# Kernel tuning notes

Hardware: AMD Instinct MI355X
Metric: run time of the kernel (lower is better)

Reference implementation:

```python
import jax, jax.numpy as jnp
import numpy as np

N_KNN = 16
BN_EPS = 1e-5


def conv1d(x, w, b):
    # x: [B, Cin, N], w: [Cout, Cin], b: [Cout] (1x1 Conv1d)
    return jnp.einsum('oc,bcn->bon', w, x) + b[None, :, None]


def conv2d(x, w, b):
    # x: [B, Cin, N, K], w: [Cout, Cin], b: [Cout] (1x1 Conv2d)
    return jnp.einsum('oc,bcnk->bonk', w, x) + b[None, :, None, None]


def bn2d(x, gamma, beta, mean, var):
    # eval-mode BatchNorm2d over channel axis 1
    scale = (gamma / jnp.sqrt(var + BN_EPS))[None, :, None, None]
    return (x - mean[None, :, None, None]) * scale + beta[None, :, None, None]


def knn_idx(pos, k):
    # pos: [B, 3, N] -> idx: [B, N, K] of k nearest neighbors (incl. self)
    p = jnp.swapaxes(pos, 1, 2)  # [B, N, 3]
    sq = jnp.sum(p * p, axis=-1)  # [B, N]
    d2 = sq[:, :, None] - 2.0 * jnp.einsum('bnd,bmd->bnm', p, p) + sq[:, None, :]
    _, idx = jax.lax.top_k(-d2, k)
    return idx


def group(x, idx):
    # x: [B, C, N], idx: [B, N, K] -> [B, C, N, K] (grouping_operation)
    return jax.vmap(lambda xb, ib: xb[:, ib])(x, idx)


def setup_inputs() -> dict:
    key = jax.random.key(0)
    B, C_OBJ, C_Q, N, DIM, PH, AM = 4, 512, 512, 4096, 128, 64, 4
    ks = jax.random.split(key, 32)
    r = lambda i, sh, s=0.05: jax.random.normal(ks[i], sh, jnp.float32) * s
    inp = {
        'obj_feature': jax.random.normal(ks[0], (B, C_OBJ, N), jnp.float32),
        'pos': jax.random.normal(ks[1], (B, 3, N), jnp.float32),
        'query_points': jax.random.normal(ks[2], (B, C_Q, N), jnp.float32),
        # linear_start_query / linear_start_obj
        'w_sq': r(3, (DIM, C_Q)), 'b_sq': r(4, (DIM,)),
        'w_so': r(5, (DIM, C_OBJ)), 'b_so': r(6, (DIM,)),
        # key / query / value 1x1 convs
        'w_k': r(7, (DIM, DIM)), 'b_k': r(8, (DIM,)),
        'w_q': r(9, (DIM, DIM)), 'b_q': r(10, (DIM,)),
        'w_v': r(11, (DIM, DIM)), 'b_v': r(12, (DIM,)),
        # pos_mlp: Conv2d(3->PH), BN, ReLU, Conv2d(PH->DIM)
        'w_p1': r(13, (PH, 3)), 'b_p1': r(14, (PH,)),
        'g_bn1': 1.0 + r(15, (PH,)), 'be_bn1': r(16, (PH,)),
        'm_bn1': r(17, (PH,)), 'v_bn1': 1.0 + 0.1 * jax.random.uniform(ks[18], (PH,), jnp.float32),
        'w_p2': r(19, (DIM, PH)), 'b_p2': r(20, (DIM,)),
        # attn_mlp: Conv2d(DIM->DIM*AM), BN, ReLU, Conv2d(DIM*AM->DIM)
        'w_a1': r(21, (DIM * AM, DIM)), 'b_a1': r(22, (DIM * AM,)),
        'g_bn2': 1.0 + r(23, (DIM * AM,)), 'be_bn2': r(24, (DIM * AM,)),
        'm_bn2': r(25, (DIM * AM,)), 'v_bn2': 1.0 + 0.1 * jax.random.uniform(ks[26], (DIM * AM,), jnp.float32),
        # linear_end
        'w_e': r(27, (C_OBJ, DIM)), 'b_e': r(28, (C_OBJ,)),
    }
    return inp


def reference(obj_feature, pos, query_points, w_sq, b_sq, w_so, b_so, w_k, b_k,
              w_q, b_q, w_v, b_v, w_p1, b_p1, g_bn1, be_bn1, m_bn1, v_bn1,
              w_p2, b_p2, w_a1, b_a1, g_bn2, be_bn2, m_bn2, v_bn2, w_e, b_e):
    qf = conv1d(query_points, w_sq, b_sq)          # [B, dim, N]
    f = conv1d(obj_feature, w_so, b_so)            # [B, dim, N]
    idx = knn_idx(jax.lax.stop_gradient(pos), N_KNN)  # [B, N, K]
    key_g = group(conv1d(f, w_k, b_k), idx)        # [B, dim, N, K]
    value = conv1d(f, w_v, b_v)                    # [B, dim, N]
    query = conv1d(qf, w_q, b_q)                   # [B, dim, N]
    qk_rel = query[:, :, :, None] - key_g          # [B, dim, N, K]
    pos_rel = pos[:, :, :, None] - group(pos, idx)  # [B, 3, N, K]
    pe = conv2d(jax.nn.relu(bn2d(conv2d(pos_rel, w_p1, b_p1), g_bn1, be_bn1, m_bn1, v_bn1)), w_p2, b_p2)
    attn = conv2d(jax.nn.relu(bn2d(conv2d(qk_rel + pe, w_a1, b_a1), g_bn2, be_bn2, m_bn2, v_bn2)), w_a2_placeholder := w_p2 * 0 + 0, b_p2 * 0) if False else None
    hidden = jax.nn.relu(bn2d(conv2d(qk_rel + pe, w_a1, b_a1), g_bn2, be_bn2, m_bn2, v_bn2))
    attn = jax.nn.softmax(conv2d(hidden, w_a2, b_a2), axis=-1)  # softmax over K
    v = value[:, :, :, None] + pe                  # [B, dim, N, K]
    agg = jnp.sum(attn * v, axis=-1)               # 'b c i j, b c i j -> b c i'
    return conv1d(agg, w_e, b_e)                   # [B, C_obj, N]

# fix: w_a2/b_a2 are parameters; re-declare reference cleanly to include them

def _setup_extra(inp):
    kk = jax.random.split(jax.random.key(7), 2)
    inp['w_a2'] = jax.random.normal(kk[0], (128, 512), jnp.float32) * 0.05
    inp['b_a2'] = jax.random.normal(kk[1], (128,), jnp.float32) * 0.05
    return inp

_orig_setup = setup_inputs

def setup_inputs():
    return _setup_extra(_orig_setup())


def reference(obj_feature, pos, query_points, w_sq, b_sq, w_so, b_so, w_k, b_k,
              w_q, b_q, w_v, b_v, w_p1, b_p1, g_bn1, be_bn1, m_bn1, v_bn1,
              w_p2, b_p2, w_a1, b_a1, g_bn2, be_bn2, m_bn2, v_bn2, w_a2, b_a2,
              w_e, b_e):
    qf = conv1d(query_points, w_sq, b_sq)
    f = conv1d(obj_feature, w_so, b_so)
    idx = knn_idx(jax.lax.stop_gradient(pos), N_KNN)
    key_g = group(conv1d(f, w_k, b_k), idx)
    value = conv1d(f, w_v, b_v)
    query = conv1d(qf, w_q, b_q)
    qk_rel = query[:, :, :, None] - key_g
    pos_rel = pos[:, :, :, None] - group(pos, idx)
    pe = conv2d(jax.nn.relu(bn2d(conv2d(pos_rel, w_p1, b_p1), g_bn1, be_bn1, m_bn1, v_bn1)), w_p2, b_p2)
    hidden = jax.nn.relu(bn2d(conv2d(qk_rel + pe, w_a1, b_a1), g_bn2, be_bn2, m_bn2, v_bn2))
    attn = jax.nn.softmax(conv2d(hidden, w_a2, b_a2), axis=-1)
    v = value[:, :, :, None] + pe
    agg = jnp.sum(attn * v, axis=-1)
    return conv1d(agg, w_e, b_e)
```

## Files before the change

### kernel.cpp

```cpp
#include <hip/hip_runtime.h>

typedef __bf16 bf16;
typedef __bf16 bf16x8 __attribute__((ext_vector_type(8)));
typedef __bf16 bf16x4 __attribute__((ext_vector_type(4)));
typedef __bf16 bf16x2 __attribute__((ext_vector_type(2)));
typedef float f32x4 __attribute__((ext_vector_type(4)));

#define MFMA16(a,b,c) __builtin_amdgcn_mfma_f32_16x16x32_bf16((a),(b),(c),0,0,0)

#define NPTS 4096
#define CIN 512
#define DIM 128
#define PH 64
#define HID 512

#define OFF_WQS 0u
#define OFF_WKO (128u*1024u)
#define OFF_WVO (256u*1024u)
#define OFF_BQS (384u*1024u)
#define OFF_BKO (385u*1024u)
#define OFF_BVO (386u*1024u)
#define OFF_S1  (387u*1024u)
#define OFF_T1  (388u*1024u)
#define OFF_S2  (389u*1024u)
#define OFF_T2  (391u*1024u)
#define OFF_CW  (400u*1024u)
#define OFF_QT  (1u<<20)
#define OFF_KT  (OFF_QT + (4u<<20))
#define OFF_VT  (OFF_QT + (8u<<20))
#define OFF_IDX (OFF_QT + (12u<<20))
#define WS_NEED (OFF_QT + (13u<<20))

struct P {
  const float* in[31];
  char* ws;
  float* out;
  int ybase;
};

template<int C> __device__ __forceinline__ float rorf(float x){
  return __int_as_float(__builtin_amdgcn_mov_dpp(__float_as_int(x), 0x120|C, 0xF, 0xF, true));
}
__device__ __forceinline__ float red16max(float x){
  x=fmaxf(x,rorf<1>(x)); x=fmaxf(x,rorf<2>(x)); x=fmaxf(x,rorf<4>(x)); x=fmaxf(x,rorf<8>(x)); return x;
}
__device__ __forceinline__ float red16sum(float x){
  x+=rorf<1>(x); x+=rorf<2>(x); x+=rorf<4>(x); x+=rorf<8>(x); return x;
}
template<int C> __device__ __forceinline__ unsigned long long ror64(unsigned long long k){
  unsigned lo = (unsigned)__builtin_amdgcn_mov_dpp((int)(unsigned)k,        0x120|C, 0xF, 0xF, true);
  unsigned hi = (unsigned)__builtin_amdgcn_mov_dpp((int)(unsigned)(k>>32), 0x120|C, 0xF, 0xF, true);
  return ((unsigned long long)hi<<32)|lo;
}

__global__ __launch_bounds__(256) void k_fold(P p) {
  int tid = blockIdx.x*256 + threadIdx.x;
  char* ws = p.ws;
  if (tid < 196608) {
    int m_id = tid >> 16, o = (tid >> 9) & 127, c = tid & 511;
    const float* A  = m_id==0 ? p.in[9] : (m_id==1 ? p.in[7] : p.in[11]);
    const float* Bm = (m_id==0) ? p.in[3] : p.in[5];
    float acc = 0.f;
    #pragma unroll 8
    for (int m=0;m<128;m++) acc += A[o*128+m] * Bm[m*512+c];
    bf16* outw = (bf16*)(ws + (m_id==0?OFF_WQS: m_id==1?OFF_WKO:OFF_WVO));
    outw[o*512+c] = (bf16)acc;
  } else if (tid < 196992) {
    int t = tid - 196608; int m_id = t >> 7, o = t & 127;
    const float* A  = m_id==0 ? p.in[9] : (m_id==1 ? p.in[7] : p.in[11]);
    const float* bb = (m_id==0) ? p.in[4] : p.in[6];
    const float* bs = m_id==0 ? p.in[10] : (m_id==1 ? p.in[8] : p.in[12]);
    float acc = bs[o];
    for (int m=0;m<128;m++) acc += A[o*128+m] * bb[m];
    float* ob = (float*)(ws + (m_id==0?OFF_BQS: m_id==1?OFF_BKO:OFF_BVO));
    ob[o] = acc;
  } else if (tid < 197056) {
    int i = tid - 196992;
    float s = p.in[15][i] * rsqrtf(p.in[18][i] + 1e-5f);
    ((float*)(ws+OFF_S1))[i] = s;
    ((float*)(ws+OFF_T1))[i] = (p.in[14][i] - p.in[17][i])*s + p.in[16][i];
  } else if (tid < 197568) {
    int i = tid - 197056;
    float s = p.in[23][i] * rsqrtf(p.in[26][i] + 1e-5f);
    ((float*)(ws+OFF_S2))[i] = s;
    ((float*)(ws+OFF_T2))[i] = (p.in[22][i] - p.in[25][i])*s + p.in[24][i];
  } else if (tid < 223168) {
    int e0 = (tid - 197568) * 8;
    const float* src; int base;
    if (e0 < 8192)        { src = p.in[19]; base = 0; }
    else if (e0 < 73728)  { src = p.in[21]; base = 8192; }
    else if (e0 < 139264) { src = p.in[29]; base = 73728; }
    else                  { src = p.in[27]; base = 139264; }
    const float* sp = src + (e0 - base);
    f32x4 a = *(const f32x4*)sp, b2 = *(const f32x4*)(sp+4);
    bf16x8 o8;
    o8[0]=(bf16)a[0]; o8[1]=(bf16)a[1]; o8[2]=(bf16)a[2]; o8[3]=(bf16)a[3];
    o8[4]=(bf16)b2[0]; o8[5]=(bf16)b2[1]; o8[6]=(bf16)b2[2]; o8[7]=(bf16)b2[3];
    *(bf16x8*)((bf16*)(ws+OFF_CW) + e0) = o8;
  }
}

__global__ __launch_bounds__(256) void k_knn(P p) {
  int lane = threadIdx.x & 63, w = threadIdx.x >> 6;
  int ig = blockIdx.x*4 + w;
  int b = ig >> 12, n = ig & 4095;
  const float* pb = p.in[1] + b*3*NPTS;
  float qx = pb[n], qy = pb[NPTS+n], qz = pb[2*NPTS+n];
  float sqn = __fadd_rn(__fadd_rn(__fmul_rn(qx,qx), __fmul_rn(qy,qy)), __fmul_rn(qz,qz));
  unsigned u[64];
  #pragma unroll
  for (int t=0;t<64;t++) {
    int j = t*64 + lane;
    float xj=pb[j], yj=pb[NPTS+j], zj=pb[2*NPTS+j];
    float sqj = __fadd_rn(__fadd_rn(__fmul_rn(xj,xj), __fmul_rn(yj,yj)), __fmul_rn(zj,zj));
    float dot = __fadd_rn(__fadd_rn(__fmul_rn(qx,xj), __fmul_rn(qy,yj)), __fmul_rn(qz,zj));
    float d2 = __fadd_rn(__fsub_rn(sqn, __fmul_rn(2.f,dot)), sqj);
    unsigned bb2 = __float_as_uint(d2);
    u[t] = bb2 ^ (((unsigned)((int)bb2 >> 31)) | 0x80000000u);
  }
  unsigned v0=u[0], v1=u[16], v2=u[32], v3=u[48];
  int t0=0, t1=16, t2=32, t3=48;
  #pragma unroll
  for (int i=1;i<16;i++) {
    { bool lt=u[i]    <v0; v0=lt?u[i]   :v0; t0=lt?(i)   :t0; }
    { bool lt=u[16+i] <v1; v1=lt?u[16+i]:v1; t1=lt?(16+i):t1; }
    { bool lt=u[32+i] <v2; v2=lt?u[32+i]:v2; t2=lt?(32+i):t2; }
    { bool lt=u[48+i] <v3; v3=lt?u[48+i]:v3; t3=lt?(48+i):t3; }
  }
  int* op = (int*)(p.ws + OFF_IDX) + ig*16;
  #pragma unroll 1
  for (int r=0;r<16;r++) {
    unsigned va=v0; int ta=t0;
    { bool lt=v1<va; va=lt?v1:va; ta=lt?t1:ta; }
    unsigned vb=v2; int tb=t2;
    { bool lt=v3<vb; vb=lt?v3:vb; tb=lt?t3:tb; }
    { bool lt=vb<va; va=lt?vb:va; ta=lt?tb:ta; }
    unsigned long long key = ((unsigned long long)va << 12) | (unsigned)((ta<<6) | lane);
    { unsigned long long o = ror64<1>(key); if (o<key) key=o; }
    { unsigned long long o = ror64<2>(key); if (o<key) key=o; }
    { unsigned long long o = ror64<4>(key); if (o<key) key=o; }
    { unsigned long long o = ror64<8>(key); if (o<key) key=o; }
    { unsigned long long o = __shfl_xor(key,16); if (o<key) key=o; }
    { unsigned long long o = __shfl_xor(key,32); if (o<key) key=o; }
    unsigned jwin = (unsigned)key & 4095u;
    if (lane==0) op[r] = (int)jwin;
    if (r==15) break;
    int tsel = __builtin_amdgcn_readfirstlane((int)(jwin>>6));
    bool mine = ((int)(jwin&63)==lane);
    switch (tsel) {
#define CLR(T) case T: u[T] = mine ? 0xFFFFFFFFu : u[T]; break;
      CLR(0) CLR(1) CLR(2) CLR(3) CLR(4) CLR(5) CLR(6) CLR(7)
      CLR(8) CLR(9) CLR(10) CLR(11) CLR(12) CLR(13) CLR(14) CLR(15)
      CLR(16) CLR(17) CLR(18) CLR(19) CLR(20) CLR(21) CLR(22) CLR(23)
      CLR(24) CLR(25) CLR(26) CLR(27) CLR(28) CLR(29) CLR(30) CLR(31)
      CLR(32) CLR(33) CLR(34) CLR(35) CLR(36) CLR(37) CLR(38) CLR(39)
      CLR(40) CLR(41) CLR(42) CLR(43) CLR(44) CLR(45) CLR(46) CLR(47)
      CLR(48) CLR(49) CLR(50) CLR(51) CLR(52) CLR(53) CLR(54) CLR(55)
      CLR(56) CLR(57) CLR(58) CLR(59) CLR(60) CLR(61) CLR(62) CLR(63)
#undef CLR
      default: break;
    }
    switch (tsel >> 4) {
      case 0: { v0=u[0]; t0=0;
        #pragma unroll
        for (int i=1;i<16;i++){ bool lt=u[i]<v0; v0=lt?u[i]:v0; t0=lt?i:t0; } } break;
      case 1: { v1=u[16]; t1=16;
        #pragma unroll
        for (int i=1;i<16;i++){ bool lt=u[16+i]<v1; v1=lt?u[16+i]:v1; t1=lt?(16+i):t1; } } break;
      case 2: { v2=u[32]; t2=32;
        #pragma unroll
        for (int i=1;i<16;i++){ bool lt=u[32+i]<v2; v2=lt?u[32+i]:v2; t2=lt?(32+i):t2; } } break;
      default: { v3=u[48]; t3=48;
        #pragma unroll
        for (int i=1;i<16;i++){ bool lt=u[48+i]<v3; v3=lt?u[48+i]:v3; t3=lt?(48+i):t3; } } break;
    }
  }
}

__global__ __launch_bounds__(256) void k_qkv(P p) {
  int mat = blockIdx.z, b = blockIdx.y, n0 = blockIdx.x*64;
  int tid = threadIdx.x, lane = tid&63, w = tid>>6;
  const float* in = (mat==0 ? p.in[2] : p.in[0]) + b*CIN*NPTS;
  const bf16* W = (const bf16*)(p.ws + (mat==0?OFF_WQS: mat==1?OFF_WKO:OFF_WVO));
  const float* bias = (const float*)(p.ws + (mat==0?OFF_BQS: mat==1?OFF_BKO:OFF_BVO));
  bf16* outT = (bf16*)(p.ws + (mat==0?OFF_QT: mat==1?OFF_KT:OFF_VT)) + (b*NPTS + n0)*DIM;
  __shared__ __align__(16) bf16 Bl[64*40];
  f32x4 acc[8] = {};
  for (int ks=0; ks<16; ks++) {
    int c0 = ks*32;
    {
      int cc = tid>>3, nn0 = (tid&7)*8;
      const float* sp = in + (c0+cc)*NPTS + n0 + nn0;
      f32x4 a = *(const f32x4*)sp, b2 = *(const f32x4*)(sp+4);
      Bl[(nn0+0)*40+cc]=(bf16)a[0];  Bl[(nn0+1)*40+cc]=(bf16)a[1];
      Bl[(nn0+2)*40+cc]=(bf16)a[2];  Bl[(nn0+3)*40+cc]=(bf16)a[3];
      Bl[(nn0+4)*40+cc]=(bf16)b2[0]; Bl[(nn0+5)*40+cc]=(bf16)b2[1];
      Bl[(nn0+6)*40+cc]=(bf16)b2[2]; Bl[(nn0+7)*40+cc]=(bf16)b2[3];
    }
    __syncthreads();
    int ncol = w*16 + (lane&15);
    bf16x8 bfr = *(const bf16x8*)(&Bl[ncol*40 + (lane>>4)*8]);
    #pragma unroll
    for (int ot=0;ot<8;ot++) {
      bf16x8 af = *(const bf16x8*)(W + (ot*16 + (lane&15))*CIN + c0 + (lane>>4)*8);
      acc[ot] = MFMA16(af, bfr, acc[ot]);
    }
    __syncthreads();
  }
  int o0 = (lane>>4)*4;
  int nloc = w*16 + (lane&15);
  #pragma unroll
  for (int ot=0;ot<8;ot++) {
    f32x4 bs = *(const f32x4*)(bias + ot*16 + o0);
    bf16x4 st;
    st[0]=(bf16)(acc[ot][0]+bs[0]); st[1]=(bf16)(acc[ot][1]+bs[1]);
    st[2]=(bf16)(acc[ot][2]+bs[2]); st[3]=(bf16)(acc[ot][3]+bs[3]);
    *(bf16x4*)(outT + nloc*DIM + ot*16 + o0) = st;
  }
}

__global__ __launch_bounds__(512) void k_fused(P p) {
  int bb = p.ybase + blockIdx.y, pt0 = blockIdx.x*8;
  int tid=threadIdx.x, lane=tid&63, w=tid>>6;
  int c = lane&15, g = lane>>4;
  char* ws = p.ws;
  const bf16* qT = (const bf16*)(ws+OFF_QT) + bb*NPTS*DIM;
  const bf16* kT = (const bf16*)(ws+OFF_KT) + bb*NPTS*DIM;
  const bf16* vT = (const bf16*)(ws+OFF_VT) + bb*NPTS*DIM;
  const int* idxg = (const int*)(ws+OFF_IDX) + (bb*NPTS + pt0)*16;
  const bf16* wp2b = (const bf16*)(ws+OFF_CW);
  const bf16* wa1b = wp2b + 8192;
  const bf16* wa2b = wa1b + 65536;
  const bf16* web  = wa2b + 65536;
  const float* s2 = (const float*)(ws+OFF_S2);
  const float* t2 = (const float*)(ws+OFF_T2);
  __shared__ __align__(16) char LB[53248];
  bf16* Xl = (bf16*)LB;
  bf16* HT = (bf16*)(LB + 34816);
  bf16* aggl = (bf16*)(LB + 34816);

  {
    int col = w*16 + c;
    int j = idxg[col] & 4095;
    const float* pb = p.in[1] + bb*3*NPTS;
    int n = pt0 + w;
    float r0 = pb[n]-pb[j], r1 = pb[NPTS+n]-pb[NPTS+j], r2 = pb[2*NPTS+n]-pb[2*NPTS+j];
    const float* wp1 = p.in[13];
    const float* s1 = (const float*)(ws+OFF_S1);
    const float* t1 = (const float*)(ws+OFF_T1);
    #pragma unroll
    for (int i=0;i<16;i+=2) {
      int m = g*16 + i;
      float x0 = wp1[m*3]*r0   + wp1[m*3+1]*r1 + wp1[m*3+2]*r2;
      float x1 = wp1[m*3+3]*r0 + wp1[m*3+4]*r1 + wp1[m*3+5]*r2;
      bf16x2 pk;
      pk[0] = (bf16)fmaxf(0.f, x0*s1[m]   + t1[m]);
      pk[1] = (bf16)fmaxf(0.f, x1*s1[m+1] + t1[m+1]);
      *(bf16x2*)(&HT[col*72 + m]) = pk;
    }
  }
  __syncthreads();

  {
    f32x4 acc[8] = {};
    int crow = w*16 + c;
    #pragma unroll
    for (int ksx=0; ksx<2; ksx++) {
      int m0 = ksx*32 + g*8;
      bf16x8 af = *(const bf16x8*)(wp2b + crow*PH + m0);
      #pragma unroll
      for (int nt=0; nt<8; nt++) {
        int col = nt*16 + c;
        bf16x8 bfr = *(const bf16x8*)(&HT[col*72 + m0]);
        acc[nt] = MFMA16(af, bfr, acc[nt]);
      }
    }
    int c0 = w*16 + g*4;
    f32x4 bp4 = *(const f32x4*)(p.in[20] + c0);
    #pragma unroll
    for (int nt=0; nt<8; nt++) {
      int col = nt*16 + c;
      int j = idxg[col] & 4095;
      int n = pt0 + nt;
      bf16x4 q4 = *(const bf16x4*)(qT + n*DIM + c0);
      bf16x4 k4 = *(const bf16x4*)(kT + j*DIM + c0);
      bf16x4 st;
      #pragma unroll
      for (int r=0;r<4;r++)
        st[r] = (bf16)((float)q4[r] - (float)k4[r] + acc[nt][r] + bp4[r]);
      *(bf16x4*)(&Xl[col*136 + c0]) = st;
    }
  }
  __syncthreads();

  int mh = w & 1, nc1 = w >> 1;
  int wo = w & 3, wc = w >> 2;
  f32x4 S[2][4] = {{{},{},{},{}},{{},{},{},{}}};
  for (int ch=0; ch<8; ch++) {
    f32x4 acc1[2][2] = {{{},{}},{{},{}}};
    #pragma unroll
    for (int ksx=0; ksx<4; ksx++) {
      int k0 = ksx*32 + g*8;
      bf16x8 af0 = *(const bf16x8*)(wa1b + (ch*64 + mh*32 + c)*DIM + k0);
      bf16x8 af1 = *(const bf16x8*)(wa1b + (ch*64 + mh*32 + 16 + c)*DIM + k0);
      bf16x8 b0  = *(const bf16x8*)(&Xl[(nc1*32 + c)*136 + k0]);
      bf16x8 b1  = *(const bf16x8*)(&Xl[(nc1*32 + 16 + c)*136 + k0]);
      acc1[0][0] = MFMA16(af0, b0, acc1[0][0]);
      acc1[0][1] = MFMA16(af0, b1, acc1[0][1]);
      acc1[1][0] = MFMA16(af1, b0, acc1[1][0]);
      acc1[1][1] = MFMA16(af1, b1, acc1[1][1]);
    }
    #pragma unroll
    for (int i2=0;i2<2;i2++) {
      int hl = mh*32 + i2*16 + g*4;
      int hg = ch*64 + hl;
      f32x4 sv = *(const f32x4*)(s2 + hg);
      f32x4 tv = *(const f32x4*)(t2 + hg);
      #pragma unroll
      for (int j2=0;j2<2;j2++) {
        int col = nc1*32 + j2*16 + c;
        bf16x4 st;
        st[0]=(bf16)fmaxf(0.f, acc1[i2][j2][0]*sv[0]+tv[0]);
        st[1]=(bf16)fmaxf(0.f, acc1[i2][j2][1]*sv[1]+tv[1]);
        st[2]=(bf16)fmaxf(0.f, acc1[i2][j2][2]*sv[2]+tv[2]);
        st[3]=(bf16)fmaxf(0.f, acc1[i2][j2][3]*sv[3]+tv[3]);
        *(bf16x4*)(&HT[col*72 + hl]) = st;
      }
    }
    __syncthreads();
    #pragma unroll
    for (int ksx=0; ksx<2; ksx++) {
      int k0 = ksx*32 + g*8;
      bf16x8 af0 = *(const bf16x8*)(wa2b + (wo*32 + c)*HID + ch*64 + k0);
      bf16x8 af1 = *(const bf16x8*)(wa2b + (wo*32 + 16 + c)*HID + ch*64 + k0);
      #pragma unroll
      for (int n2=0;n2<4;n2++) {
        bf16x8 bfr = *(const bf16x8*)(&HT[(wc*64 + n2*16 + c)*72 + k0]);
        S[0][n2] = MFMA16(af0, bfr, S[0][n2]);
        S[1][n2] = MFMA16(af1, bfr, S[1][n2]);
      }
    }
    __syncthreads();
  }

  {
    #pragma unroll
    for (int n2=0;n2<4;n2++) {
      int ptl = wc*4 + n2;
      int colg = ptl*16 + c;
      int j = idxg[colg] & 4095;
      int n = pt0 + ptl;
      #pragma unroll
      for (int i2=0;i2<2;i2++) {
        int chb = wo*32 + i2*16 + g*4;
        bf16x4 x4 = *(const bf16x4*)(&Xl[colg*136 + chb]);
        bf16x4 q4 = *(const bf16x4*)(qT + n*DIM + chb);
        bf16x4 k4 = *(const bf16x4*)(kT + j*DIM + chb);
        bf16x4 v4 = *(const bf16x4*)(vT + n*DIM + chb);
        float agv[4];
        #pragma unroll
        for (int r=0;r<4;r++) {
          float s = S[i2][n2][r];
          float mx = red16max(s);
          float e = __expf(s-mx);
          float sm = red16sum(e);
          float at = e/sm;
          float vpe = (float)v4[r] + (float)x4[r] - (float)q4[r] + (float)k4[r];
          agv[r] = red16sum(at*vpe);
        }
        if (c==0) {
          bf16x4 st; st[0]=(bf16)agv[0]; st[1]=(bf16)agv[1]; st[2]=(bf16)agv[2]; st[3]=(bf16)agv[3];
          *(bf16x4*)(&aggl[ptl*136 + chb]) = st;
        }
      }
    }
  }
  __syncthreads();

  {
    const float* be = p.in[28];
    f32x4 acc5[4] = {};
    #pragma unroll
    for (int ksx=0; ksx<4; ksx++) {
      bf16x8 bfr = *(const bf16x8*)(&aggl[c*136 + ksx*32 + g*8]);
      #pragma unroll
      for (int i=0;i<4;i++) {
        int e = (w*4+i)*16 + c;
        bf16x8 af = *(const bf16x8*)(web + e*DIM + ksx*32 + g*8);
        acc5[i] = MFMA16(af, bfr, acc5[i]);
      }
    }
    if (c < 8) {
      int n = pt0 + c;
      #pragma unroll
      for (int i=0;i<4;i++) {
        int e0 = (w*4+i)*16 + g*4;
        f32x4 be4 = *(const f32x4*)(be + e0);
        #pragma unroll
        for (int r=0;r<4;r++)
          p.out[(bb*CIN + e0+r)*NPTS + n] = acc5[i][r] + be4[r];
      }
    }
  }
}

extern "C" void kernel_launch(void* const* d_in, const int* in_sizes, int n_in,
                              void* d_out, int out_size, void* d_ws, size_t ws_size,
                              hipStream_t stream) {
  if (ws_size < WS_NEED || n_in < 31) return;
  P p;
  for (int i=0;i<31;i++) p.in[i] = (const float*)d_in[i];
  p.ws = (char*)d_ws;
  p.out = (float*)d_out;
  p.ybase = 0;
  k_fold<<<872, 256, 0, stream>>>(p);
  k_knn<<<4096, 256, 0, stream>>>(p);
  k_qkv<<<dim3(64, 4, 3), 256, 0, stream>>>(p);
  k_fused<<<dim3(512, 4), 512, 0, stream>>>(p);
}
```

Measured before the change: 476.0 us.

## Merge knn and qkv launches; halve fused tile to 4 points per block

The qkv projection blocks are folded into the knn kernel as a leading range of block indices, so both independent jobs share one launch and can overlap on the device. The fused attention kernel now handles 4 points (64 neighbor columns) per block instead of 8, with a reworked warp-to-tile mapping, 128-wide hidden chunks and a smaller LDS footprint (about 33KB instead of 52KB). This raises block count and occupancy, at the cost of loading the weights again for every block, twice as often overall.

```diff
diff --git a/kernel.cpp b/kernel.cpp
--- a/kernel.cpp
+++ b/kernel.cpp
@@ -100,9 +100,52 @@
   }
 }
 
-__global__ __launch_bounds__(256) void k_knn(P p) {
+__global__ __launch_bounds__(256) void k_knnqkv(P p) {
+  if (blockIdx.x < 768) {
+    int qb = blockIdx.x;
+    int mat = qb >> 8, b = (qb >> 6) & 3, n0 = (qb & 63) * 64;
+    int tid = threadIdx.x, lane = tid&63, w = tid>>6;
+    const float* in = (mat==0 ? p.in[2] : p.in[0]) + b*CIN*NPTS;
+    const bf16* W = (const bf16*)(p.ws + (mat==0?OFF_WQS: mat==1?OFF_WKO:OFF_WVO));
+    const float* bias = (const float*)(p.ws + (mat==0?OFF_BQS: mat==1?OFF_BKO:OFF_BVO));
+    bf16* outT = (bf16*)(p.ws + (mat==0?OFF_QT: mat==1?OFF_KT:OFF_VT)) + (b*NPTS + n0)*DIM;
+    __shared__ __align__(16) bf16 Bl[64*40];
+    f32x4 acc[8] = {};
+    for (int ks=0; ks<16; ks++) {
+      int c0 = ks*32;
+      {
+        int cc = tid>>3, nn0 = (tid&7)*8;
+        const float* sp = in + (c0+cc)*NPTS + n0 + nn0;
+        f32x4 a = *(const f32x4*)sp, b2 = *(const f32x4*)(sp+4);
+        Bl[(nn0+0)*40+cc]=(bf16)a[0];  Bl[(nn0+1)*40+cc]=(bf16)a[1];
+        Bl[(nn0+2)*40+cc]=(bf16)a[2];  Bl[(nn0+3)*40+cc]=(bf16)a[3];
+        Bl[(nn0+4)*40+cc]=(bf16)b2[0]; Bl[(nn0+5)*40+cc]=(bf16)b2[1];
+        Bl[(nn0+6)*40+cc]=(bf16)b2[2]; Bl[(nn0+7)*40+cc]=(bf16)b2[3];
+      }
+      __syncthreads();
+      int ncol = w*16 + (lane&15);
+      bf16x8 bfr = *(const bf16x8*)(&Bl[ncol*40 + (lane>>4)*8]);
+      #pragma unroll
+      for (int ot=0;ot<8;ot++) {
+        bf16x8 af = *(const bf16x8*)(W + (ot*16 + (lane&15))*CIN + c0 + (lane>>4)*8);
+        acc[ot] = MFMA16(af, bfr, acc[ot]);
+      }
+      __syncthreads();
+    }
+    int o0 = (lane>>4)*4;
+    int nloc = w*16 + (lane&15);
+    #pragma unroll
+    for (int ot=0;ot<8;ot++) {
+      f32x4 bs = *(const f32x4*)(bias + ot*16 + o0);
+      bf16x4 st;
+      st[0]=(bf16)(acc[ot][0]+bs[0]); st[1]=(bf16)(acc[ot][1]+bs[1]);
+      st[2]=(bf16)(acc[ot][2]+bs[2]); st[3]=(bf16)(acc[ot][3]+bs[3]);
+      *(bf16x4*)(outT + nloc*DIM + ot*16 + o0) = st;
+    }
+    return;
+  }
   int lane = threadIdx.x & 63, w = threadIdx.x >> 6;
-  int ig = blockIdx.x*4 + w;
+  int ig = (blockIdx.x - 768)*4 + w;
   int b = ig >> 12, n = ig & 4095;
   const float* pb = p.in[1] + b*3*NPTS;
   float qx = pb[n], qy = pb[NPTS+n], qz = pb[2*NPTS+n];
@@ -177,50 +220,8 @@
   }
 }
 
-__global__ __launch_bounds__(256) void k_qkv(P p) {
-  int mat = blockIdx.z, b = blockIdx.y, n0 = blockIdx.x*64;
-  int tid = threadIdx.x, lane = tid&63, w = tid>>6;
-  const float* in = (mat==0 ? p.in[2] : p.in[0]) + b*CIN*NPTS;
-  const bf16* W = (const bf16*)(p.ws + (mat==0?OFF_WQS: mat==1?OFF_WKO:OFF_WVO));
-  const float* bias = (const float*)(p.ws + (mat==0?OFF_BQS: mat==1?OFF_BKO:OFF_BVO));
-  bf16* outT = (bf16*)(p.ws + (mat==0?OFF_QT: mat==1?OFF_KT:OFF_VT)) + (b*NPTS + n0)*DIM;
-  __shared__ __align__(16) bf16 Bl[64*40];
-  f32x4 acc[8] = {};
-  for (int ks=0; ks<16; ks++) {
-    int c0 = ks*32;
-    {
-      int cc = tid>>3, nn0 = (tid&7)*8;
-      const float* sp = in + (c0+cc)*NPTS + n0 + nn0;
-      f32x4 a = *(const f32x4*)sp, b2 = *(const f32x4*)(sp+4);
-      Bl[(nn0+0)*40+cc]=(bf16)a[0];  Bl[(nn0+1)*40+cc]=(bf16)a[1];
-      Bl[(nn0+2)*40+cc]=(bf16)a[2];  Bl[(nn0+3)*40+cc]=(bf16)a[3];
-      Bl[(nn0+4)*40+cc]=(bf16)b2[0]; Bl[(nn0+5)*40+cc]=(bf16)b2[1];
-      Bl[(nn0+6)*40+cc]=(bf16)b2[2]; Bl[(nn0+7)*40+cc]=(bf16)b2[3];
-    }
-    __syncthreads();
-    int ncol = w*16 + (lane&15);
-    bf16x8 bfr = *(const bf16x8*)(&Bl[ncol*40 + (lane>>4)*8]);
-    #pragma unroll
-    for (int ot=0;ot<8;ot++) {
-      bf16x8 af = *(const bf16x8*)(W + (ot*16 + (lane&15))*CIN + c0 + (lane>>4)*8);
-      acc[ot] = MFMA16(af, bfr, acc[ot]);
-    }
-    __syncthreads();
-  }
-  int o0 = (lane>>4)*4;
-  int nloc = w*16 + (lane&15);
-  #pragma unroll
-  for (int ot=0;ot<8;ot++) {
-    f32x4 bs = *(const f32x4*)(bias + ot*16 + o0);
-    bf16x4 st;
-    st[0]=(bf16)(acc[ot][0]+bs[0]); st[1]=(bf16)(acc[ot][1]+bs[1]);
-    st[2]=(bf16)(acc[ot][2]+bs[2]); st[3]=(bf16)(acc[ot][3]+bs[3]);
-    *(bf16x4*)(outT + nloc*DIM + ot*16 + o0) = st;
-  }
-}
-
 __global__ __launch_bounds__(512) void k_fused(P p) {
-  int bb = p.ybase + blockIdx.y, pt0 = blockIdx.x*8;
+  int bb = blockIdx.y, pt0 = blockIdx.x*4;
   int tid=threadIdx.x, lane=tid&63, w=tid>>6;
   int c = lane&15, g = lane>>4;
   char* ws = p.ws;
@@ -234,144 +235,139 @@
   const bf16* web  = wa2b + 65536;
   const float* s2 = (const float*)(ws+OFF_S2);
   const float* t2 = (const float*)(ws+OFF_T2);
-  __shared__ __align__(16) char LB[53248];
+  __shared__ __align__(16) char LB[33792];
   bf16* Xl = (bf16*)LB;
-  bf16* HT = (bf16*)(LB + 34816);
-  bf16* aggl = (bf16*)(LB + 34816);
+  bf16* HT = (bf16*)(LB + 16896);
+  bf16* aggl = (bf16*)(LB + 16896);
 
   {
-    int col = w*16 + c;
+    int col = lane;
     int j = idxg[col] & 4095;
     const float* pb = p.in[1] + bb*3*NPTS;
-    int n = pt0 + w;
+    int n = pt0 + (col>>4);
     float r0 = pb[n]-pb[j], r1 = pb[NPTS+n]-pb[NPTS+j], r2 = pb[2*NPTS+n]-pb[2*NPTS+j];
     const float* wp1 = p.in[13];
     const float* s1 = (const float*)(ws+OFF_S1);
     const float* t1 = (const float*)(ws+OFF_T1);
-    #pragma unroll
-    for (int i=0;i<16;i+=2) {
-      int m = g*16 + i;
-      float x0 = wp1[m*3]*r0   + wp1[m*3+1]*r1 + wp1[m*3+2]*r2;
-      float x1 = wp1[m*3+3]*r0 + wp1[m*3+4]*r1 + wp1[m*3+5]*r2;
-      bf16x2 pk;
-      pk[0] = (bf16)fmaxf(0.f, x0*s1[m]   + t1[m]);
-      pk[1] = (bf16)fmaxf(0.f, x1*s1[m+1] + t1[m+1]);
-      *(bf16x2*)(&HT[col*72 + m]) = pk;
-    }
+    bf16x4 o4[2];
+    #pragma unroll
+    for (int i=0;i<8;i++) {
+      int m = w*8 + i;
+      float x = wp1[m*3]*r0 + wp1[m*3+1]*r1 + wp1[m*3+2]*r2;
+      o4[i>>2][i&3] = (bf16)fmaxf(0.f, x*s1[m] + t1[m]);
+    }
+    *(bf16x4*)(&HT[col*132 + w*8])     = o4[0];
+    *(bf16x4*)(&HT[col*132 + w*8 + 4]) = o4[1];
   }
   __syncthreads();
 
   {
-    f32x4 acc[8] = {};
-    int crow = w*16 + c;
+    f32x4 acc[4] = {};
+    int erow = w*16 + c;
     #pragma unroll
     for (int ksx=0; ksx<2; ksx++) {
       int m0 = ksx*32 + g*8;
-      bf16x8 af = *(const bf16x8*)(wp2b + crow*PH + m0);
-      #pragma unroll
-      for (int nt=0; nt<8; nt++) {
-        int col = nt*16 + c;
-        bf16x8 bfr = *(const bf16x8*)(&HT[col*72 + m0]);
-        acc[nt] = MFMA16(af, bfr, acc[nt]);
+      bf16x8 af = *(const bf16x8*)(wp2b + erow*PH + m0);
+      #pragma unroll
+      for (int ct=0; ct<4; ct++) {
+        bf16x8 bfr = *(const bf16x8*)(&HT[(ct*16+c)*132 + m0]);
+        acc[ct] = MFMA16(af, bfr, acc[ct]);
       }
     }
     int c0 = w*16 + g*4;
     f32x4 bp4 = *(const f32x4*)(p.in[20] + c0);
     #pragma unroll
-    for (int nt=0; nt<8; nt++) {
-      int col = nt*16 + c;
+    for (int ct=0; ct<4; ct++) {
+      int col = ct*16 + c;
       int j = idxg[col] & 4095;
-      int n = pt0 + nt;
+      int n = pt0 + ct;
       bf16x4 q4 = *(const bf16x4*)(qT + n*DIM + c0);
       bf16x4 k4 = *(const bf16x4*)(kT + j*DIM + c0);
       bf16x4 st;
       #pragma unroll
       for (int r=0;r<4;r++)
-        st[r] = (bf16)((float)q4[r] - (float)k4[r] + acc[nt][r] + bp4[r]);
-      *(bf16x4*)(&Xl[col*136 + c0]) = st;
+        st[r] = (bf16)((float)q4[r] - (float)k4[r] + acc[ct][r] + bp4[r]);
+      *(bf16x4*)(&Xl[col*132 + c0]) = st;
     }
   }
   __syncthreads();
 
-  int mh = w & 1, nc1 = w >> 1;
-  int wo = w & 3, wc = w >> 2;
-  f32x4 S[2][4] = {{{},{},{},{}},{{},{},{},{}}};
-  for (int ch=0; ch<8; ch++) {
-    f32x4 acc1[2][2] = {{{},{}},{{},{}}};
+  int wh = w >> 1, wc1 = w & 1;
+  f32x4 S[2][2] = {{{},{}},{{},{}}};
+  for (int ch=0; ch<4; ch++) {
+    f32x4 a1[2][2] = {{{},{}},{{},{}}};
     #pragma unroll
     for (int ksx=0; ksx<4; ksx++) {
       int k0 = ksx*32 + g*8;
-      bf16x8 af0 = *(const bf16x8*)(wa1b + (ch*64 + mh*32 + c)*DIM + k0);
-      bf16x8 af1 = *(const bf16x8*)(wa1b + (ch*64 + mh*32 + 16 + c)*DIM + k0);
-      bf16x8 b0  = *(const bf16x8*)(&Xl[(nc1*32 + c)*136 + k0]);
-      bf16x8 b1  = *(const bf16x8*)(&Xl[(nc1*32 + 16 + c)*136 + k0]);
-      acc1[0][0] = MFMA16(af0, b0, acc1[0][0]);
-      acc1[0][1] = MFMA16(af0, b1, acc1[0][1]);
-      acc1[1][0] = MFMA16(af1, b0, acc1[1][0]);
-      acc1[1][1] = MFMA16(af1, b1, acc1[1][1]);
+      bf16x8 af0 = *(const bf16x8*)(wa1b + (ch*128 + wh*32 + c)*DIM + k0);
+      bf16x8 af1 = *(const bf16x8*)(wa1b + (ch*128 + wh*32 + 16 + c)*DIM + k0);
+      bf16x8 b0  = *(const bf16x8*)(&Xl[(wc1*32 + c)*132 + k0]);
+      bf16x8 b1  = *(const bf16x8*)(&Xl[(wc1*32 + 16 + c)*132 + k0]);
+      a1[0][0] = MFMA16(af0, b0, a1[0][0]);
+      a1[0][1] = MFMA16(af0, b1, a1[0][1]);
+      a1[1][0] = MFMA16(af1, b0, a1[1][0]);
+      a1[1][1] = MFMA16(af1, b1, a1[1][1]);
     }
     #pragma unroll
     for (int i2=0;i2<2;i2++) {
-      int hl = mh*32 + i2*16 + g*4;
-      int hg = ch*64 + hl;
+      int hl = wh*32 + i2*16 + g*4;
+      int hg = ch*128 + hl;
       f32x4 sv = *(const f32x4*)(s2 + hg);
       f32x4 tv = *(const f32x4*)(t2 + hg);
       #pragma unroll
       for (int j2=0;j2<2;j2++) {
-        int col = nc1*32 + j2*16 + c;
+        int col = wc1*32 + j2*16 + c;
         bf16x4 st;
-        st[0]=(bf16)fmaxf(0.f, acc1[i2][j2][0]*sv[0]+tv[0]);
-        st[1]=(bf16)fmaxf(0.f, acc1[i2][j2][1]*sv[1]+tv[1]);
-        st[2]=(bf16)fmaxf(0.f, acc1[i2][j2][2]*sv[2]+tv[2]);
-        st[3]=(bf16)fmaxf(0.f, acc1[i2][j2][3]*sv[3]+tv[3]);
-        *(bf16x4*)(&HT[col*72 + hl]) = st;
+        st[0]=(bf16)fmaxf(0.f, a1[i2][j2][0]*sv[0]+tv[0]);
+        st[1]=(bf16)fmaxf(0.f, a1[i2][j2][1]*sv[1]+tv[1]);
+        st[2]=(bf16)fmaxf(0.f, a1[i2][j2][2]*sv[2]+tv[2]);
+        st[3]=(bf16)fmaxf(0.f, a1[i2][j2][3]*sv[3]+tv[3]);
+        *(bf16x4*)(&HT[col*132 + hl]) = st;
       }
     }
     __syncthreads();
     #pragma unroll
-    for (int ksx=0; ksx<2; ksx++) {
-      int k0 = ksx*32 + g*8;
-      bf16x8 af0 = *(const bf16x8*)(wa2b + (wo*32 + c)*HID + ch*64 + k0);
-      bf16x8 af1 = *(const bf16x8*)(wa2b + (wo*32 + 16 + c)*HID + ch*64 + k0);
-      #pragma unroll
-      for (int n2=0;n2<4;n2++) {
-        bf16x8 bfr = *(const bf16x8*)(&HT[(wc*64 + n2*16 + c)*72 + k0]);
-        S[0][n2] = MFMA16(af0, bfr, S[0][n2]);
-        S[1][n2] = MFMA16(af1, bfr, S[1][n2]);
-      }
+    for (int ksg=0; ksg<4; ksg++) {
+      int k0 = ksg*32 + g*8;
+      bf16x8 af0 = *(const bf16x8*)(wa2b + (wh*32 + c)*HID + ch*128 + k0);
+      bf16x8 af1 = *(const bf16x8*)(wa2b + (wh*32 + 16 + c)*HID + ch*128 + k0);
+      bf16x8 b0  = *(const bf16x8*)(&HT[(wc1*32 + c)*132 + k0]);
+      bf16x8 b1  = *(const bf16x8*)(&HT[(wc1*32 + 16 + c)*132 + k0]);
+      S[0][0] = MFMA16(af0, b0, S[0][0]);
+      S[0][1] = MFMA16(af0, b1, S[0][1]);
+      S[1][0] = MFMA16(af1, b0, S[1][0]);
+      S[1][1] = MFMA16(af1, b1, S[1][1]);
     }
     __syncthreads();
   }
 
-  {
-    #pragma unroll
-    for (int n2=0;n2<4;n2++) {
-      int ptl = wc*4 + n2;
+  #pragma unroll
+  for (int i2=0;i2<2;i2++) {
+    #pragma unroll
+    for (int j2=0;j2<2;j2++) {
+      int ptl = wc1*2 + j2;
       int colg = ptl*16 + c;
       int j = idxg[colg] & 4095;
       int n = pt0 + ptl;
-      #pragma unroll
-      for (int i2=0;i2<2;i2++) {
-        int chb = wo*32 + i2*16 + g*4;
-        bf16x4 x4 = *(const bf16x4*)(&Xl[colg*136 + chb]);
-        bf16x4 q4 = *(const bf16x4*)(qT + n*DIM + chb);
-        bf16x4 k4 = *(const bf16x4*)(kT + j*DIM + chb);
-        bf16x4 v4 = *(const bf16x4*)(vT + n*DIM + chb);
-        float agv[4];
-        #pragma unroll
-        for (int r=0;r<4;r++) {
-          float s = S[i2][n2][r];
-          float mx = red16max(s);
-          float e = __expf(s-mx);
-          float sm = red16sum(e);
-          float at = e/sm;
-          float vpe = (float)v4[r] + (float)x4[r] - (float)q4[r] + (float)k4[r];
-          agv[r] = red16sum(at*vpe);
-        }
-        if (c==0) {
-          bf16x4 st; st[0]=(bf16)agv[0]; st[1]=(bf16)agv[1]; st[2]=(bf16)agv[2]; st[3]=(bf16)agv[3];
-          *(bf16x4*)(&aggl[ptl*136 + chb]) = st;
-        }
+      int chb = wh*32 + i2*16 + g*4;
+      bf16x4 x4 = *(const bf16x4*)(&Xl[colg*132 + chb]);
+      bf16x4 q4 = *(const bf16x4*)(qT + n*DIM + chb);
+      bf16x4 k4 = *(const bf16x4*)(kT + j*DIM + chb);
+      bf16x4 v4 = *(const bf16x4*)(vT + n*DIM + chb);
+      float agv[4];
+      #pragma unroll
+      for (int r=0;r<4;r++) {
+        float s = S[i2][j2][r];
+        float mx = red16max(s);
+        float e = __expf(s-mx);
+        float sm = red16sum(e);
+        float at = e/sm;
+        float vpe = (float)v4[r] + (float)x4[r] - (float)q4[r] + (float)k4[r];
+        agv[r] = red16sum(at*vpe);
+      }
+      if (c==0) {
+        bf16x4 st; st[0]=(bf16)agv[0]; st[1]=(bf16)agv[1]; st[2]=(bf16)agv[2]; st[3]=(bf16)agv[3];
+        *(bf16x4*)(&aggl[ptl*132 + chb]) = st;
       }
     }
   }
@@ -382,7 +378,7 @@
     f32x4 acc5[4] = {};
     #pragma unroll
     for (int ksx=0; ksx<4; ksx++) {
-      bf16x8 bfr = *(const bf16x8*)(&aggl[c*136 + ksx*32 + g*8]);
+      bf16x8 bfr = *(const bf16x8*)(&aggl[c*132 + ksx*32 + g*8]);
       #pragma unroll
       for (int i=0;i<4;i++) {
         int e = (w*4+i)*16 + c;
@@ -390,7 +386,7 @@
         acc5[i] = MFMA16(af, bfr, acc5[i]);
       }
     }
-    if (c < 8) {
+    if (c < 4) {
       int n = pt0 + c;
       #pragma unroll
       for (int i=0;i<4;i++) {
@@ -414,7 +410,6 @@
   p.out = (float*)d_out;
   p.ybase = 0;
   k_fold<<<872, 256, 0, stream>>>(p);
-  k_knn<<<4096, 256, 0, stream>>>(p);
-  k_qkv<<<dim3(64, 4, 3), 256, 0, stream>>>(p);
-  k_fused<<<dim3(512, 4), 512, 0, stream>>>(p);
-}
+  k_knnqkv<<<768 + 4096, 256, 0, stream>>>(p);
+  k_fused<<<dim3(1024, 4), 512, 0, stream>>>(p);
+}
```

New measurement: 584.2 us. 1.23x slower.
